# Optimization experiments

Hardware: AMD Instinct MI355X
Metric: run time of the kernel (lower is better)

Reference implementation:

```python
import jax, jax.numpy as jnp
import numpy as np

SIZE_IN = 1024
SIZE_OUT = 1024
N_ROWS = 16384
MAX_VAL = 127.0  # nemo=False -> int8 path


def _quantize(t, max_val):
    """Per-tensor symmetric quantization matching the torch code.
    scale = max_val / max(|min(t)|, |max(t)|) (1.0 if t_max==0);
    q = clamp(round(scale*t), -max_val, max_val) cast to int8."""
    t_max = jnp.maximum(jnp.abs(jnp.min(t)), jnp.abs(jnp.max(t)))
    t_max = jnp.where(t_max == 0.0, 1.0, t_max)
    scale = max_val / t_max
    q = jnp.clip(jnp.round(scale * t), -max_val, max_val).astype(jnp.int8)
    return q, scale


def setup_inputs() -> dict:
    key = jax.random.key(0)
    kx, kw, kb = jax.random.split(key, 3)
    x = jax.random.normal(kx, (N_ROWS, SIZE_IN), dtype=jnp.float32)
    # kaiming_uniform_(a=sqrt(5)) -> uniform(-1/sqrt(fan_in), 1/sqrt(fan_in))
    bound = 1.0 / np.sqrt(SIZE_IN)
    weight = jax.random.uniform(kw, (SIZE_OUT, SIZE_IN), dtype=jnp.float32,
                                minval=-bound, maxval=bound)
    bias = jax.random.uniform(kb, (SIZE_OUT,), dtype=jnp.float32,
                              minval=-bound, maxval=bound)
    return {"x": x, "weight": weight, "bias": bias}


def reference(x, weight, bias):
    qw, sw = _quantize(weight, MAX_VAL)          # [SIZE_OUT, SIZE_IN] int8
    qx, sa = _quantize(x, MAX_VAL)               # [N, SIZE_IN] int8
    qb, sb = _quantize(bias, MAX_VAL)            # [SIZE_OUT] int8
    # for the approximate axx kernel), then dequantize.
    acc = jnp.matmul(qx.astype(jnp.int32), qw.astype(jnp.int32).T)  # [N, SIZE_OUT]
    out = acc.astype(jnp.float32) / (sa * sw)
    out = out + qb.astype(jnp.float32) / sb
    return out
```

## Files before the change

kernel.cpp:

```cpp
#include <hip/hip_runtime.h>


#define M_ROWS 16384
#define K_DIM  1024
#define N_OUT  1024

typedef int v4i __attribute__((ext_vector_type(4)));
typedef float v4f __attribute__((ext_vector_type(4)));

__device__ __forceinline__ void gload_lds16(const void* g, void* l) {
  __builtin_amdgcn_global_load_lds(
      (const __attribute__((address_space(1))) void*)g,
      (__attribute__((address_space(3))) void*)l, 16, 0, 0);
}

__device__ __forceinline__ float block_reduce_max4(float m, float* red) {
#pragma unroll
  for (int off = 32; off > 0; off >>= 1)
    m = fmaxf(m, __shfl_down(m, off));
  const int wid = threadIdx.x >> 6, lane = threadIdx.x & 63;
  if (lane == 0) red[wid] = m;
  __syncthreads();
  float r = fmaxf(fmaxf(red[0], red[1]), fmaxf(red[2], red[3]));
  __syncthreads();
  return r;
}

__global__ void amax_stage1(const float* __restrict__ src, int n4,
                            float* __restrict__ partials) {
  __shared__ float red[4];
  float m = 0.0f;
  const int stride = gridDim.x * blockDim.x;
  for (int idx = blockIdx.x * blockDim.x + threadIdx.x; idx < n4; idx += stride) {
    float4 v = ((const float4*)src)[idx];
    m = fmaxf(m, fmaxf(fmaxf(fabsf(v.x), fabsf(v.y)), fmaxf(fabsf(v.z), fabsf(v.w))));
  }
  float r = block_reduce_max4(m, red);
  if (threadIdx.x == 0) partials[blockIdx.x] = r;
}

__global__ void finalize_kernel(const float* __restrict__ px, int npx,
                                const float* __restrict__ pw, int npw,
                                const float* __restrict__ bias,
                                float* __restrict__ amax,
                                float* __restrict__ bdeq) {
  __shared__ float red[4];
  const int tid = threadIdx.x;

  float m = 0.0f;
  for (int i = tid; i < npx; i += 256) m = fmaxf(m, px[i]);
  float rx = block_reduce_max4(m, red);

  m = 0.0f;
  for (int i = tid; i < npw; i += 256) m = fmaxf(m, pw[i]);
  float rw = block_reduce_max4(m, red);

  float4 bv = ((const float4*)bias)[tid];
  m = fmaxf(fmaxf(fabsf(bv.x), fabsf(bv.y)), fmaxf(fabsf(bv.z), fabsf(bv.w)));
  float rb = block_reduce_max4(m, red);

  if (rx == 0.0f) rx = 1.0f;
  if (rw == 0.0f) rw = 1.0f;
  if (rb == 0.0f) rb = 1.0f;
  if (tid == 0) {
    amax[0] = rx;
    amax[1] = rw;
    amax[2] = rb;
  }
  const float sb = 127.0f / rb;
  float4 q;
  q.x = fminf(fmaxf(rintf(sb * bv.x), -127.0f), 127.0f) / sb;
  q.y = fminf(fmaxf(rintf(sb * bv.y), -127.0f), 127.0f) / sb;
  q.z = fminf(fmaxf(rintf(sb * bv.z), -127.0f), 127.0f) / sb;
  q.w = fminf(fmaxf(rintf(sb * bv.w), -127.0f), 127.0f) / sb;
  ((float4*)bdeq)[tid] = q;
}

__global__ void quant_kernel(const float* __restrict__ src, signed char* __restrict__ dst,
                             int n4, const float* __restrict__ amax, int slot) {
  const float s = 127.0f / amax[slot];
  const int stride = gridDim.x * blockDim.x;
  for (int idx = blockIdx.x * blockDim.x + threadIdx.x; idx < n4; idx += stride) {
    float4 v = ((const float4*)src)[idx];
    int q0 = (int)fminf(fmaxf(rintf(s * v.x), -127.0f), 127.0f);
    int q1 = (int)fminf(fmaxf(rintf(s * v.y), -127.0f), 127.0f);
    int q2 = (int)fminf(fmaxf(rintf(s * v.z), -127.0f), 127.0f);
    int q3 = (int)fminf(fmaxf(rintf(s * v.w), -127.0f), 127.0f);
    unsigned int packed = (q0 & 0xff) | ((q1 & 0xff) << 8) |
                          ((q2 & 0xff) << 16) | ((q3 & 0xff) << 24);
    ((unsigned int*)dst)[idx] = packed;
  }
}

#define NKT 16

__global__ __launch_bounds__(256, 2) void gemm_kernel(
    const signed char* __restrict__ qx, const signed char* __restrict__ qw,
    const float* __restrict__ amax, const float* __restrict__ bdeq,
    float* __restrict__ out) {
  __shared__ char lds[49152];

  const int tid  = threadIdx.x;
  const int w    = tid >> 6;
  const int lane = tid & 63;
  const int wm = w >> 1;
  const int wn = w & 1;
  const int fr = lane & 15;
  const int q  = lane >> 4;

  const int bid = blockIdx.x;
  const int wg  = (bid & 7) * 64 + (bid >> 3);
  const int Mbase = (wg >> 3) * 256;
  const int Nbase = (wg & 7) * 128;

  const signed char* gA = qx + (size_t)Mbase * K_DIM;
  const signed char* gB = qw + (size_t)Nbase * K_DIM;

  const int srow = tid >> 2;
  const int scol = ((tid & 3) ^ ((tid >> 3) & 3)) << 4;

  const int u0    = (q ^ ((fr >> 1) & 3)) << 4;
  const int aoffA = fr * 64 + u0;
  const int aoffB = fr * 64 + u0;

  const float inv_denom = (amax[0] * amax[1]) * (1.0f / 16129.0f);
  float bdq[4];
#pragma unroll
  for (int g = 0; g < 4; ++g) bdq[g] = bdeq[Nbase + wn * 64 + g * 16 + fr];

  v4i acc[8][4] = {};
  v4i Ar[8], Br[4];

#define STG(BUF, T)                                                            \
  do {                                                                         \
    const int _k0 = (T)*64 + scol;                                             \
    char* _la = lds + (BUF)*24576;                                             \
    char* _lb = _la + 16384;                                                   \
    _Pragma("unroll") for (int i = 0; i < 4; ++i)                              \
      gload_lds16(gA + (size_t)(i * 64 + srow) * K_DIM + _k0,                  \
                  _la + i * 4096 + tid * 16);                                  \
    _Pragma("unroll") for (int i = 0; i < 2; ++i)                              \
      gload_lds16(gB + (size_t)(i * 64 + srow) * K_DIM + _k0,                  \
                  _lb + i * 4096 + tid * 16);                                  \
  } while (0)

#define VM(N) asm volatile("s_waitcnt vmcnt(" #N ")" ::: "memory")

  STG(0, 0);
  int cur = 0;
  for (int kt = 0; kt < NKT; ++kt) {
    if (kt + 1 < NKT) {
      STG(cur ^ 1, kt + 1);
      VM(6);
    } else {
      VM(0);
    }
    __builtin_amdgcn_s_barrier();

    const char* _A = lds + cur * 24576 + wm * 8192;
    const char* _B = lds + cur * 24576 + 16384 + wn * 4096;
#pragma unroll
    for (int f = 0; f < 8; ++f)
      Ar[f] = *(const v4i*)(_A + aoffA + f * 1024);
#pragma unroll
    for (int g = 0; g < 4; ++g)
      Br[g] = *(const v4i*)(_B + aoffB + g * 1024);
#pragma unroll
    for (int f = 0; f < 8; ++f)
#pragma unroll
      for (int g = 0; g < 4; ++g)
        acc[f][g] = __builtin_amdgcn_mfma_i32_16x16x64_i8(Ar[f], Br[g], acc[f][g], 0, 0, 0);

    asm volatile("s_waitcnt lgkmcnt(0)" ::: "memory");
    __builtin_amdgcn_s_barrier();
    cur ^= 1;
  }
#undef STG
#undef VM

  __syncthreads();

  float* lws = (float*)(lds + w * 12288);

  const int erow = lane >> 4;
  const int ecg  = lane & 15;
  float* const orow_base = out + (size_t)(Mbase + wm * 128) * N_OUT +
                           (Nbase + wn * 64) + ecg * 4;

#pragma unroll
  for (int f = 0; f < 8; ++f) {
#pragma unroll
    for (int g = 0; g < 4; ++g)
#pragma unroll
      for (int i = 0; i < 4; ++i)
        lws[(q * 4 + i) * 66 + g * 16 + fr] =
            (float)acc[f][g][i] * inv_denom + bdq[g];
    asm volatile("s_waitcnt lgkmcnt(0)" ::: "memory");
#pragma unroll
    for (int t = 0; t < 4; ++t) {
      const int r16 = t * 4 + erow;
      v4f v = *(const v4f*)&lws[r16 * 66 + ecg * 4];
      __builtin_nontemporal_store(
          v, (v4f*)(orow_base + (size_t)(f * 16 + r16) * N_OUT));
    }
    asm volatile("s_waitcnt lgkmcnt(0)" ::: "memory");
  }
}

extern "C" void kernel_launch(void* const* d_in, const int* in_sizes, int n_in,
                              void* d_out, int out_size, void* d_ws, size_t ws_size,
                              hipStream_t stream) {
  const float* x = (const float*)d_in[0];
  const float* w = (const float*)d_in[1];
  const float* b = (const float*)d_in[2];
  float* out = (float*)d_out;

  char* ws = (char*)d_ws;
  float* amax = (float*)ws;
  float* bdeq = (float*)(ws + 256);
  float* px   = (float*)(ws + 8192);
  float* pw   = (float*)(ws + 16384 + 8192);
  signed char* qw = (signed char*)(ws + 65536);
  signed char* qx = (signed char*)(ws + (1 << 21));

  const int NPX = 2048, NPW = 256;
  hipLaunchKernelGGL(amax_stage1, dim3(NPX), dim3(256), 0, stream, x, M_ROWS * K_DIM / 4, px);
  hipLaunchKernelGGL(amax_stage1, dim3(NPW), dim3(256), 0, stream, w, N_OUT * K_DIM / 4, pw);
  hipLaunchKernelGGL(finalize_kernel, dim3(1), dim3(256), 0, stream, px, NPX, pw, NPW, b, amax, bdeq);
  hipLaunchKernelGGL(quant_kernel, dim3(2048), dim3(256), 0, stream, x, qx, M_ROWS * K_DIM / 4, amax, 0);
  hipLaunchKernelGGL(quant_kernel, dim3(256), dim3(256), 0, stream, w, qw, N_OUT * K_DIM / 4, amax, 1);
  hipLaunchKernelGGL(gemm_kernel, dim3(128 * 4), dim3(256), 0, stream, qx, qw, amax, bdeq, out);
}
```

Baseline: 65.53 us.

## Restructure int8 GEMM main loop into quadrant-split 8-wave-style ping-pong pipeline

Replaces the simple double-buffered K loop with a finer-grained schedule. Each K tile's MFMA work is split into four 4x2 quadrants, and the LDS reads and async global-to-LDS loads for halves of A and B are interleaved between them, with s_setprio raised around the MFMA bursts. The aim is to hide the LDS read and global load latency behind matrix work and shrink register pressure from the A/B fragments. The cost is many extra barriers per tile and a delicate ordering of vmcnt waits and buffer reuse, which could cause stalls or races.

```diff
diff --git a/kernel.cpp b/kernel.cpp
--- a/kernel.cpp
+++ b/kernel.cpp
@@ -116,71 +116,101 @@
   const signed char* gA = qx + (size_t)Mbase * K_DIM;
   const signed char* gB = qw + (size_t)Nbase * K_DIM;
 
-  const int srow = tid >> 2;
   const int scol = ((tid & 3) ^ ((tid >> 3) & 3)) << 4;
-
-  const int u0    = (q ^ ((fr >> 1) & 3)) << 4;
-  const int aoffA = fr * 64 + u0;
-  const int aoffB = fr * 64 + u0;
+  const int u0b  = (q ^ ((fr >> 1) & 3)) << 4;
 
   const float inv_denom = (amax[0] * amax[1]) * (1.0f / 16129.0f);
-  float bdq[4];
-#pragma unroll
-  for (int g = 0; g < 4; ++g) bdq[g] = bdeq[Nbase + wn * 64 + g * 16 + fr];
 
   v4i acc[8][4] = {};
-  v4i Ar[8], Br[4];
-
-#define STG(BUF, T)                                                            \
+  v4i Ar[4];
+  v4i Br[2][2];
+
+#define STG_A(BUF, H, T)                                                       \
   do {                                                                         \
     const int _k0 = (T)*64 + scol;                                             \
-    char* _la = lds + (BUF)*24576;                                             \
-    char* _lb = _la + 16384;                                                   \
-    _Pragma("unroll") for (int i = 0; i < 4; ++i)                              \
-      gload_lds16(gA + (size_t)(i * 64 + srow) * K_DIM + _k0,                  \
-                  _la + i * 4096 + tid * 16);                                  \
-    _Pragma("unroll") for (int i = 0; i < 2; ++i)                              \
-      gload_lds16(gB + (size_t)(i * 64 + srow) * K_DIM + _k0,                  \
-                  _lb + i * 4096 + tid * 16);                                  \
+    char* _l = lds + (BUF)*24576 + (H)*8192 + tid * 16;                        \
+    const signed char* _g = gA + (size_t)((H)*128 + (tid >> 2)) * K_DIM + _k0; \
+    gload_lds16(_g, _l);                                                       \
+    gload_lds16(_g + (size_t)64 * K_DIM, _l + 4096);                           \
+  } while (0)
+
+#define STG_B(BUF, H, T)                                                       \
+  do {                                                                         \
+    const int _k0 = (T)*64 + scol;                                             \
+    gload_lds16(gB + (size_t)((H)*64 + (tid >> 2)) * K_DIM + _k0,              \
+                lds + (BUF)*24576 + 16384 + (H)*4096 + tid * 16);              \
+  } while (0)
+
+#define RD_A(BUF, MH)                                                          \
+  do {                                                                         \
+    const char* _A = lds + (BUF)*24576 + wm * 8192 + (MH)*4096;                \
+    _Pragma("unroll") for (int f = 0; f < 4; ++f)                              \
+        Ar[f] = *(const v4i*)(_A + f * 1024 + fr * 64 + u0b);                  \
+  } while (0)
+
+#define RD_B(BUF, NH)                                                          \
+  do {                                                                         \
+    const char* _B = lds + (BUF)*24576 + 16384 + wn * 4096 + (NH)*2048;        \
+    _Pragma("unroll") for (int g = 0; g < 2; ++g)                              \
+        Br[NH][g] = *(const v4i*)(_B + g * 1024 + fr * 64 + u0b);              \
+  } while (0)
+
+#define MFMA_Q(MH, NH)                                                         \
+  do {                                                                         \
+    __builtin_amdgcn_s_setprio(1);                                             \
+    _Pragma("unroll") for (int f = 0; f < 4; ++f)                              \
+      _Pragma("unroll") for (int g = 0; g < 2; ++g)                            \
+          acc[(MH)*4 + f][(NH)*2 + g] = __builtin_amdgcn_mfma_i32_16x16x64_i8( \
+              Ar[f], Br[NH][g], acc[(MH)*4 + f][(NH)*2 + g], 0, 0, 0);         \
+    __builtin_amdgcn_s_setprio(0);                                             \
   } while (0)
 
 #define VM(N) asm volatile("s_waitcnt vmcnt(" #N ")" ::: "memory")
-
-  STG(0, 0);
-  int cur = 0;
-  for (int kt = 0; kt < NKT; ++kt) {
-    if (kt + 1 < NKT) {
-      STG(cur ^ 1, kt + 1);
-      VM(6);
-    } else {
-      VM(0);
-    }
-    __builtin_amdgcn_s_barrier();
-
-    const char* _A = lds + cur * 24576 + wm * 8192;
-    const char* _B = lds + cur * 24576 + 16384 + wn * 4096;
-#pragma unroll
-    for (int f = 0; f < 8; ++f)
-      Ar[f] = *(const v4i*)(_A + aoffA + f * 1024);
-#pragma unroll
-    for (int g = 0; g < 4; ++g)
-      Br[g] = *(const v4i*)(_B + aoffB + g * 1024);
-#pragma unroll
-    for (int f = 0; f < 8; ++f)
-#pragma unroll
-      for (int g = 0; g < 4; ++g)
-        acc[f][g] = __builtin_amdgcn_mfma_i32_16x16x64_i8(Ar[f], Br[g], acc[f][g], 0, 0, 0);
-
-    asm volatile("s_waitcnt lgkmcnt(0)" ::: "memory");
-    __builtin_amdgcn_s_barrier();
-    cur ^= 1;
-  }
-#undef STG
-#undef VM
-
+#define LGKM0() asm volatile("s_waitcnt lgkmcnt(0)" ::: "memory")
+#define BAR() __builtin_amdgcn_s_barrier()
+
+  STG_B(0, 0, 0); STG_B(0, 1, 0); STG_A(0, 0, 0); STG_A(0, 1, 0);
+  STG_B(1, 0, 1); STG_B(1, 1, 1); STG_A(1, 0, 1);
+  VM(4);
+  BAR();
+
+  for (int j = 0; j < 8; ++j) {
+    const int tb1 = (2 * j + 1) & 15;
+    const int t2  = (2 * j + 2) & 15;
+    const int t3  = (2 * j + 3) & 15;
+    RD_A(0, 0); RD_B(0, 0); STG_A(1, 1, tb1);
+    BAR(); LGKM0(); MFMA_Q(0, 0); BAR();
+    RD_B(0, 1);
+    BAR(); LGKM0(); MFMA_Q(0, 1); BAR();
+    RD_A(0, 1); STG_B(0, 0, t2);
+    BAR(); LGKM0(); MFMA_Q(1, 1); BAR();
+    STG_B(0, 1, t2);
+    BAR(); MFMA_Q(1, 0); VM(2); BAR();
+    RD_A(1, 0); RD_B(1, 0); STG_A(0, 0, t2);
+    BAR(); LGKM0(); MFMA_Q(0, 0); BAR();
+    RD_B(1, 1); STG_A(0, 1, t2);
+    BAR(); LGKM0(); MFMA_Q(0, 1); BAR();
+    RD_A(1, 1); STG_B(1, 0, t3);
+    BAR(); LGKM0(); MFMA_Q(1, 1); BAR();
+    STG_B(1, 1, t3); STG_A(1, 0, t3);
+    BAR(); MFMA_Q(1, 0); VM(4); BAR();
+  }
+#undef STG_A
+#undef STG_B
+#undef RD_A
+#undef RD_B
+#undef MFMA_Q
+
+  VM(0);
   __syncthreads();
 
-  float* lws = (float*)(lds + w * 12288);
+  const float bdq0 = bdeq[Nbase + wn * 64 + fr];
+  const float bdq1 = bdeq[Nbase + wn * 64 + 16 + fr];
+  const float bdq2 = bdeq[Nbase + wn * 64 + 32 + fr];
+  const float bdq3 = bdeq[Nbase + wn * 64 + 48 + fr];
+  const float bdq[4] = {bdq0, bdq1, bdq2, bdq3};
+
+  float* lws = (float*)(lds + w * 8192);
 
   const int erow = lane >> 4;
   const int ecg  = lane & 15;
@@ -190,21 +220,25 @@
 #pragma unroll
   for (int f = 0; f < 8; ++f) {
 #pragma unroll
-    for (int g = 0; g < 4; ++g)
+    for (int g = 0; g < 4; ++g) {
+      const int lc = (g >> 1) * 32 + (g & 1) * 16 + fr;
 #pragma unroll
       for (int i = 0; i < 4; ++i)
-        lws[(q * 4 + i) * 66 + g * 16 + fr] =
-            (float)acc[f][g][i] * inv_denom + bdq[g];
-    asm volatile("s_waitcnt lgkmcnt(0)" ::: "memory");
+        lws[(q * 4 + i) * 66 + lc] = (float)acc[f][g][i] * inv_denom + bdq[g];
+    }
+    LGKM0();
 #pragma unroll
     for (int t = 0; t < 4; ++t) {
       const int r16 = t * 4 + erow;
       v4f v = *(const v4f*)&lws[r16 * 66 + ecg * 4];
-      __builtin_nontemporal_store(
-          v, (v4f*)(orow_base + (size_t)(f * 16 + r16) * N_OUT));
+      const int row = (f >> 2) * 64 + (f & 3) * 16 + r16;
+      __builtin_nontemporal_store(v, (v4f*)(orow_base + (size_t)row * N_OUT));
     }
-    asm volatile("s_waitcnt lgkmcnt(0)" ::: "memory");
-  }
+    LGKM0();
+  }
+#undef VM
+#undef LGKM0
+#undef BAR
 }
 
 extern "C" void kernel_launch(void* const* d_in, const int* in_sizes, int n_in,
```

Result: no change. 64.54 us (-1.5%).

## Merge amax and quant launches; load GEMM operands directly from global memory

Applied to the files above, without the earlier changes.

The x and w amax reductions now run in one launch, and so do the two quantization passes, which cuts the number of kernel launches. The GEMM no longer stages operands through double-buffered LDS with barriers. Each wave reads its A and B fragments straight from global memory into registers, and LDS shrinks to a small epilogue buffer. This removes LDS staging and barrier cost. In exchange, every wave re-reads overlapping tiles from global memory or cache with no explicit prefetch, so load latency may no longer be hidden.

```diff
diff --git a/kernel.cpp b/kernel.cpp
--- a/kernel.cpp
+++ b/kernel.cpp
@@ -7,12 +7,6 @@
 
 typedef int v4i __attribute__((ext_vector_type(4)));
 typedef float v4f __attribute__((ext_vector_type(4)));
-
-__device__ __forceinline__ void gload_lds16(const void* g, void* l) {
-  __builtin_amdgcn_global_load_lds(
-      (const __attribute__((address_space(1))) void*)g,
-      (__attribute__((address_space(3))) void*)l, 16, 0, 0);
-}
 
 __device__ __forceinline__ float block_reduce_max4(float m, float* red) {
 #pragma unroll
@@ -26,17 +20,22 @@
   return r;
 }
 
-__global__ void amax_stage1(const float* __restrict__ src, int n4,
-                            float* __restrict__ partials) {
+__global__ void amax_both(const float* __restrict__ x, const float* __restrict__ wsrc,
+                          float* __restrict__ px, float* __restrict__ pw) {
   __shared__ float red[4];
+  const bool isx = blockIdx.x < 2048;
+  const float* src = isx ? x : wsrc;
+  const int n4   = isx ? (M_ROWS * K_DIM / 4) : (N_OUT * K_DIM / 4);
+  const int nblk = isx ? 2048 : 256;
+  const int bidl = isx ? blockIdx.x : blockIdx.x - 2048;
   float m = 0.0f;
-  const int stride = gridDim.x * blockDim.x;
-  for (int idx = blockIdx.x * blockDim.x + threadIdx.x; idx < n4; idx += stride) {
+  const int stride = nblk * 256;
+  for (int idx = bidl * 256 + threadIdx.x; idx < n4; idx += stride) {
     float4 v = ((const float4*)src)[idx];
     m = fmaxf(m, fmaxf(fmaxf(fabsf(v.x), fabsf(v.y)), fmaxf(fabsf(v.z), fabsf(v.w))));
   }
   float r = block_reduce_max4(m, red);
-  if (threadIdx.x == 0) partials[blockIdx.x] = r;
+  if (threadIdx.x == 0) (isx ? px : pw)[bidl] = r;
 }
 
 __global__ void finalize_kernel(const float* __restrict__ px, int npx,
@@ -76,11 +75,18 @@
   ((float4*)bdeq)[tid] = q;
 }
 
-__global__ void quant_kernel(const float* __restrict__ src, signed char* __restrict__ dst,
-                             int n4, const float* __restrict__ amax, int slot) {
-  const float s = 127.0f / amax[slot];
-  const int stride = gridDim.x * blockDim.x;
-  for (int idx = blockIdx.x * blockDim.x + threadIdx.x; idx < n4; idx += stride) {
+__global__ void quant_both(const float* __restrict__ x, const float* __restrict__ wsrc,
+                           signed char* __restrict__ qx, signed char* __restrict__ qw,
+                           const float* __restrict__ amax) {
+  const bool isx = blockIdx.x < 2048;
+  const float* src = isx ? x : wsrc;
+  signed char* dst = isx ? qx : qw;
+  const int n4   = isx ? (M_ROWS * K_DIM / 4) : (N_OUT * K_DIM / 4);
+  const int nblk = isx ? 2048 : 256;
+  const int bidl = isx ? blockIdx.x : blockIdx.x - 2048;
+  const float s = 127.0f / amax[isx ? 0 : 1];
+  const int stride = nblk * 256;
+  for (int idx = bidl * 256 + threadIdx.x; idx < n4; idx += stride) {
     float4 v = ((const float4*)src)[idx];
     int q0 = (int)fminf(fmaxf(rintf(s * v.x), -127.0f), 127.0f);
     int q1 = (int)fminf(fmaxf(rintf(s * v.y), -127.0f), 127.0f);
@@ -98,7 +104,7 @@
     const signed char* __restrict__ qx, const signed char* __restrict__ qw,
     const float* __restrict__ amax, const float* __restrict__ bdeq,
     float* __restrict__ out) {
-  __shared__ char lds[49152];
+  __shared__ char lds[4 * 4352];
 
   const int tid  = threadIdx.x;
   const int w    = tid >> 6;
@@ -113,74 +119,35 @@
   const int Mbase = (wg >> 3) * 256;
   const int Nbase = (wg & 7) * 128;
 
-  const signed char* gA = qx + (size_t)Mbase * K_DIM;
-  const signed char* gB = qw + (size_t)Nbase * K_DIM;
-
-  const int srow = tid >> 2;
-  const int scol = ((tid & 3) ^ ((tid >> 3) & 3)) << 4;
-
-  const int u0    = (q ^ ((fr >> 1) & 3)) << 4;
-  const int aoffA = fr * 64 + u0;
-  const int aoffB = fr * 64 + u0;
+  const signed char* pa = qx + (size_t)(Mbase + wm * 128 + fr) * K_DIM + q * 16;
+  const signed char* pb = qw + (size_t)(Nbase + wn * 64 + fr) * K_DIM + q * 16;
 
   const float inv_denom = (amax[0] * amax[1]) * (1.0f / 16129.0f);
-  float bdq[4];
-#pragma unroll
-  for (int g = 0; g < 4; ++g) bdq[g] = bdeq[Nbase + wn * 64 + g * 16 + fr];
 
   v4i acc[8][4] = {};
-  v4i Ar[8], Br[4];
 
-#define STG(BUF, T)                                                            \
-  do {                                                                         \
-    const int _k0 = (T)*64 + scol;                                             \
-    char* _la = lds + (BUF)*24576;                                             \
-    char* _lb = _la + 16384;                                                   \
-    _Pragma("unroll") for (int i = 0; i < 4; ++i)                              \
-      gload_lds16(gA + (size_t)(i * 64 + srow) * K_DIM + _k0,                  \
-                  _la + i * 4096 + tid * 16);                                  \
-    _Pragma("unroll") for (int i = 0; i < 2; ++i)                              \
-      gload_lds16(gB + (size_t)(i * 64 + srow) * K_DIM + _k0,                  \
-                  _lb + i * 4096 + tid * 16);                                  \
-  } while (0)
-
-#define VM(N) asm volatile("s_waitcnt vmcnt(" #N ")" ::: "memory")
-
-  STG(0, 0);
-  int cur = 0;
+#pragma unroll 2
   for (int kt = 0; kt < NKT; ++kt) {
-    if (kt + 1 < NKT) {
-      STG(cur ^ 1, kt + 1);
-      VM(6);
-    } else {
-      VM(0);
-    }
-    __builtin_amdgcn_s_barrier();
-
-    const char* _A = lds + cur * 24576 + wm * 8192;
-    const char* _B = lds + cur * 24576 + 16384 + wn * 4096;
+    const int ko = kt * 64;
+    v4i Ar[8], Br[4];
 #pragma unroll
     for (int f = 0; f < 8; ++f)
-      Ar[f] = *(const v4i*)(_A + aoffA + f * 1024);
+      Ar[f] = *(const v4i*)(pa + (size_t)f * 16 * K_DIM + ko);
 #pragma unroll
     for (int g = 0; g < 4; ++g)
-      Br[g] = *(const v4i*)(_B + aoffB + g * 1024);
+      Br[g] = *(const v4i*)(pb + (size_t)g * 16 * K_DIM + ko);
 #pragma unroll
     for (int f = 0; f < 8; ++f)
 #pragma unroll
       for (int g = 0; g < 4; ++g)
         acc[f][g] = __builtin_amdgcn_mfma_i32_16x16x64_i8(Ar[f], Br[g], acc[f][g], 0, 0, 0);
+  }
 
-    asm volatile("s_waitcnt lgkmcnt(0)" ::: "memory");
-    __builtin_amdgcn_s_barrier();
-    cur ^= 1;
-  }
-#undef STG
-#undef VM
+  float bdq[4];
+#pragma unroll
+  for (int g = 0; g < 4; ++g) bdq[g] = bdeq[Nbase + wn * 64 + g * 16 + fr];
 
-  __syncthreads();
-
-  float* lws = (float*)(lds + w * 12288);
+  float* lws = (float*)(lds + w * 4352);
 
   const int erow = lane >> 4;
   const int ecg  = lane & 15;
@@ -224,10 +191,8 @@
   signed char* qx = (signed char*)(ws + (1 << 21));
 
   const int NPX = 2048, NPW = 256;
-  hipLaunchKernelGGL(amax_stage1, dim3(NPX), dim3(256), 0, stream, x, M_ROWS * K_DIM / 4, px);
-  hipLaunchKernelGGL(amax_stage1, dim3(NPW), dim3(256), 0, stream, w, N_OUT * K_DIM / 4, pw);
+  hipLaunchKernelGGL(amax_both, dim3(NPX + NPW), dim3(256), 0, stream, x, w, px, pw);
   hipLaunchKernelGGL(finalize_kernel, dim3(1), dim3(256), 0, stream, px, NPX, pw, NPW, b, amax, bdeq);
-  hipLaunchKernelGGL(quant_kernel, dim3(2048), dim3(256), 0, stream, x, qx, M_ROWS * K_DIM / 4, amax, 0);
-  hipLaunchKernelGGL(quant_kernel, dim3(256), dim3(256), 0, stream, w, qw, N_OUT * K_DIM / 4, amax, 1);
+  hipLaunchKernelGGL(quant_both, dim3(NPX + NPW), dim3(256), 0, stream, x, w, qx, qw, amax);
   hipLaunchKernelGGL(gemm_kernel, dim3(128 * 4), dim3(256), 0, stream, qx, qw, amax, bdeq, out);
 }
```

Measured after the change: 88.74 us. 1.35x slower.
